# Optimization experiments

Measured on AMD Instinct MI355X. Metric: run time of the kernel, lower is better.

The kernel has to match this reference:

```python
import jax, jax.numpy as jnp
import numpy as np

BINARY_K = 64  # self.binary_k


def setup_inputs() -> dict:
    key = jax.random.key(0)
    ks = jax.random.split(key, 8)
    R, N, D, H = 8, 128, 512, 256
    obj_feats = jax.random.normal(ks[0], (R, N, D), dtype=jnp.float32)
    geo_feats = jax.random.normal(ks[1], (R, N, N, D), dtype=jnp.float32) * 0.1
    mask = jnp.ones((N, N), dtype=jnp.float32)
    mask = mask.at[jnp.arange(N), jnp.arange(N)].set(0.0)  # zero diagonal, as in forward()
    s1 = 1.0 / np.sqrt(D)
    s2 = 1.0 / np.sqrt(H)
    return {
        "obj_feats": obj_feats,
        "geo_feats": geo_feats,
        "mask": mask,
        "w1a": jax.random.normal(ks[2], (D, H), dtype=jnp.float32) * s1,
        "b1a": jnp.zeros((H,), dtype=jnp.float32),
        "w2a": jax.random.normal(ks[3], (H, 1), dtype=jnp.float32) * s2,
        "b2a": jnp.zeros((1,), dtype=jnp.float32),
        "w1b": jax.random.normal(ks[4], (D, H), dtype=jnp.float32) * s1,
        "b1b": jnp.zeros((H,), dtype=jnp.float32),
        "w2b": jax.random.normal(ks[5], (H, 1), dtype=jnp.float32) * s2,
        "b2b": jnp.zeros((1,), dtype=jnp.float32),
    }


def reference(obj_feats, geo_feats, mask, w1a, b1a, w2a, b2a, w1b, b1b, w2b, b2b):
    # pair_aware_perbatch (dropout = identity in eval mode)
    R, N, D = obj_feats.shape
    k = min(BINARY_K, N * N)

    # pairwise outer-product features + geometric features: [R, N, N, D]
    obj2obj = obj_feats[:, None, :, :] * obj_feats[:, :, None, :] + geo_feats

    # re_clf1 MLP scorer: D -> D/2 -> 1
    h = jax.nn.relu(jnp.einsum('rijd,dh->rijh', obj2obj, w1a) + b1a)
    logits = jnp.einsum('rijh,h->rij', h, w2a[:, 0]) + b2a[0]     # [R, N, N]
    o2o_logits = logits.reshape(R, N * N).sum(axis=0) / R          # [N*N]

    pair_probs = jax.nn.sigmoid(o2o_logits) * mask.ravel()
    _, topk_inds = jax.lax.top_k(pair_probs, k)                    # [k]

    # averaged pair features, gather topk
    a_obj2obj = obj2obj.reshape(R, N * N, D).sum(axis=0) / R       # [N*N, D]
    pair_feats = a_obj2obj[topk_inds]                              # [k, D]

    # pair-of-pair outer product + second MLP scorer
    p2p = pair_feats[None, :, :] * pair_feats[:, None, :]          # [k, k, D]
    h2 = jax.nn.relu(jnp.einsum('ijd,dh->ijh', p2p, w1b) + b1b)
    p2p_logits = jnp.einsum('ijh,h->ij', h2, w2b[:, 0]) + b2b[0]   # [k, k]

    return o2o_logits.reshape(N, N), p2p_logits, topk_inds
```

## Files before the change

kernel.cpp:

```cpp
#include <hip/hip_runtime.h>
#include <math.h>

typedef unsigned int u32;
typedef unsigned long long u64;
typedef unsigned short u16;
typedef short bf16x8 __attribute__((ext_vector_type(8)));
typedef float f32x4 __attribute__((ext_vector_type(4)));

#define RR 8
#define NN 128
#define DD 512
#define HH 256
#define KTOP 64
#define NCAND 256
#define NSEL 128

#define WS_LOGITS_OFF 0
#define WS_CAND_OFF   65536
#define WS_EXACT_OFF  66560
#define WS_CNT_OFF    67584
#define WS_TOPK_OFF   67600
#define WS_PF_OFF     67856
#define WS_WH_OFF     198928
#define WS_WL_OFF     461072

__device__ __forceinline__ u16 bf16rne(float x) {
    union { float f; u32 u; } v; v.f = x;
    u32 r = (v.u + 0x7fffu + ((v.u >> 16) & 1u)) >> 16;
    return (u16)r;
}
__device__ __forceinline__ float bf16tof(u16 h) {
    union { float f; u32 u; } v; v.u = ((u32)h) << 16; return v.f;
}
__device__ __forceinline__ u32 f32sort(float x) {
    union { float f; u32 u; } v; v.f = x;
    return v.u ^ ((v.u & 0x80000000u) ? 0xFFFFFFFFu : 0x80000000u);
}

__global__ __launch_bounds__(256) void k0_splitW(const float* __restrict__ W1,
                                                 u16* __restrict__ wh, u16* __restrict__ wl)
{
    const int kc = blockIdx.x;
    const int h  = threadIdx.x;
    const int swz = (h >> 1) & 3;
    u16 rh[32], rl[32];
#pragma unroll
    for (int kk = 0; kk < 32; ++kk) {
        float a = W1[(size_t)(kc * 32 + kk) * HH + h];
        u16 hi = bf16rne(a);
        float lo = a - bf16tof(hi);
        rh[kk] = hi; rl[kk] = bf16rne(lo);
    }
    const size_t base = (size_t)kc * 8192 + (size_t)h * 32;
#pragma unroll
    for (int q = 0; q < 4; ++q) {
        uint4 ph, pl;
        ph.x = (u32)rh[q*8+0] | ((u32)rh[q*8+1] << 16);
        ph.y = (u32)rh[q*8+2] | ((u32)rh[q*8+3] << 16);
        ph.z = (u32)rh[q*8+4] | ((u32)rh[q*8+5] << 16);
        ph.w = (u32)rh[q*8+6] | ((u32)rh[q*8+7] << 16);
        pl.x = (u32)rl[q*8+0] | ((u32)rl[q*8+1] << 16);
        pl.y = (u32)rl[q*8+2] | ((u32)rl[q*8+3] << 16);
        pl.z = (u32)rl[q*8+4] | ((u32)rl[q*8+5] << 16);
        pl.w = (u32)rl[q*8+6] | ((u32)rl[q*8+7] << 16);
        const int qs = (q ^ swz) * 8;
        *(uint4*)&wh[base + qs] = ph;
        *(uint4*)&wl[base + qs] = pl;
    }
}

__global__ __launch_bounds__(256, 2) void k1_pair_mfma(
    const float* __restrict__ obj, const float* __restrict__ geo,
    const u16* __restrict__ wh, const u16* __restrict__ wl,
    const float* __restrict__ b1, const float* __restrict__ w2,
    float* __restrict__ logits_acc)
{
    const int jb = blockIdx.x, i = blockIdx.y, r = blockIdx.z;
    const int j0 = jb * 64;
    const int tid = threadIdx.x;
    const int lane = tid & 63, wv = tid >> 6;
    const int l15 = lane & 15, quad = lane >> 4;
    const int fsl = (quad ^ ((l15 >> 1) & 3)) * 8;

    __shared__ float sObjI[DD];
    __shared__ __align__(16) u16 sAh[64 * 32], sAl[64 * 32];
    __shared__ __align__(16) u16 sBh[256 * 32], sBl[256 * 32];

    const float* objI = obj + (size_t)(r * NN + i) * DD;
    for (int t = tid; t < DD; t += 256) sObjI[t] = objI[t];

    f32x4 acc[4][4];
#pragma unroll
    for (int mt = 0; mt < 4; ++mt)
#pragma unroll
        for (int nt = 0; nt < 4; ++nt) acc[mt][nt] = (f32x4){0.f, 0.f, 0.f, 0.f};

    const float* geoB = geo + ((size_t)(r * NN + i) * NN + j0) * DD;
    const float* objJ = obj + (size_t)(r * NN + j0) * DD;

    const int aj = tid >> 2;
    const int ak = (tid & 3) * 8;
    const int asl = ((tid & 3) ^ ((aj >> 1) & 3)) * 8;

    for (int kc = 0; kc < 16; ++kc) {
        const int k0 = kc * 32;
        __syncthreads();
        {
            const char* gh = (const char*)(wh + (size_t)kc * 8192);
            const char* gl = (const char*)(wl + (size_t)kc * 8192);
#pragma unroll
            for (int p = 0; p < 4; ++p) {
                const int off = (wv * 4 + p) * 1024;
                __builtin_amdgcn_global_load_lds(
                    (const __attribute__((address_space(1))) u32*)(gh + off + lane * 16),
                    (__attribute__((address_space(3))) u32*)((char*)sBh + off), 16, 0, 0);
                __builtin_amdgcn_global_load_lds(
                    (const __attribute__((address_space(1))) u32*)(gl + off + lane * 16),
                    (__attribute__((address_space(3))) u32*)((char*)sBl + off), 16, 0, 0);
            }
        }
        {
            float4 g0 = *(const float4*)(geoB + (size_t)aj * DD + k0 + ak);
            float4 g1 = *(const float4*)(geoB + (size_t)aj * DD + k0 + ak + 4);
            float4 o0 = *(const float4*)(objJ + (size_t)aj * DD + k0 + ak);
            float4 o1 = *(const float4*)(objJ + (size_t)aj * DD + k0 + ak + 4);
            float a[8];
            a[0] = fmaf(sObjI[k0+ak+0], o0.x, g0.x);
            a[1] = fmaf(sObjI[k0+ak+1], o0.y, g0.y);
            a[2] = fmaf(sObjI[k0+ak+2], o0.z, g0.z);
            a[3] = fmaf(sObjI[k0+ak+3], o0.w, g0.w);
            a[4] = fmaf(sObjI[k0+ak+4], o1.x, g1.x);
            a[5] = fmaf(sObjI[k0+ak+5], o1.y, g1.y);
            a[6] = fmaf(sObjI[k0+ak+6], o1.z, g1.z);
            a[7] = fmaf(sObjI[k0+ak+7], o1.w, g1.w);
            u16 hs[8], ls[8];
#pragma unroll
            for (int q = 0; q < 8; ++q) {
                hs[q] = bf16rne(a[q]);
                ls[q] = bf16rne(a[q] - bf16tof(hs[q]));
            }
            uint4 ph, pl;
            ph.x = (u32)hs[0] | ((u32)hs[1] << 16); ph.y = (u32)hs[2] | ((u32)hs[3] << 16);
            ph.z = (u32)hs[4] | ((u32)hs[5] << 16); ph.w = (u32)hs[6] | ((u32)hs[7] << 16);
            pl.x = (u32)ls[0] | ((u32)ls[1] << 16); pl.y = (u32)ls[2] | ((u32)ls[3] << 16);
            pl.z = (u32)ls[4] | ((u32)ls[5] << 16); pl.w = (u32)ls[6] | ((u32)ls[7] << 16);
            *(uint4*)&sAh[aj * 32 + asl] = ph;
            *(uint4*)&sAl[aj * 32 + asl] = pl;
        }
        __syncthreads();
        bf16x8 Bh[4], Bl[4], Ah[4], Al[4];
#pragma unroll
        for (int nt = 0; nt < 4; ++nt) {
            const int row = wv * 64 + nt * 16 + l15;
            Bh[nt] = *(const bf16x8*)&sBh[row * 32 + fsl];
            Bl[nt] = *(const bf16x8*)&sBl[row * 32 + fsl];
        }
#pragma unroll
        for (int mt = 0; mt < 4; ++mt) {
            const int row = mt * 16 + l15;
            Ah[mt] = *(const bf16x8*)&sAh[row * 32 + fsl];
            Al[mt] = *(const bf16x8*)&sAl[row * 32 + fsl];
        }
#pragma unroll
        for (int mt = 0; mt < 4; ++mt)
#pragma unroll
            for (int nt = 0; nt < 4; ++nt) {
                acc[mt][nt] = __builtin_amdgcn_mfma_f32_16x16x32_bf16(Ah[mt], Bh[nt], acc[mt][nt], 0, 0, 0);
                acc[mt][nt] = __builtin_amdgcn_mfma_f32_16x16x32_bf16(Ah[mt], Bl[nt], acc[mt][nt], 0, 0, 0);
                acc[mt][nt] = __builtin_amdgcn_mfma_f32_16x16x32_bf16(Al[mt], Bh[nt], acc[mt][nt], 0, 0, 0);
            }
    }
    float pr[4][4];
#pragma unroll
    for (int mt = 0; mt < 4; ++mt)
#pragma unroll
        for (int t = 0; t < 4; ++t) pr[mt][t] = 0.f;
#pragma unroll
    for (int nt = 0; nt < 4; ++nt) {
        const int h = wv * 64 + nt * 16 + l15;
        const float bb = b1[h], w = w2[h];
#pragma unroll
        for (int mt = 0; mt < 4; ++mt)
#pragma unroll
            for (int t = 0; t < 4; ++t)
                pr[mt][t] += fmaxf(acc[mt][nt][t] + bb, 0.f) * w;
    }
#pragma unroll
    for (int mt = 0; mt < 4; ++mt)
#pragma unroll
        for (int t = 0; t < 4; ++t) {
            float v = pr[mt][t];
            v += __shfl_xor(v, 1); v += __shfl_xor(v, 2);
            v += __shfl_xor(v, 4); v += __shfl_xor(v, 8);
            if (l15 == 0)
                atomicAdd(&logits_acc[i * NN + j0 + mt * 16 + quad * 4 + t], v);
        }
}

__global__ __launch_bounds__(1024) void k2_hist(
    const float* __restrict__ logits_acc, const float* __restrict__ mask,
    const float* __restrict__ b2a, float* __restrict__ out,
    int* __restrict__ cand, int* __restrict__ cnt_out)
{
    __shared__ u32 hist[16 * 256];
    __shared__ u32 sum1[256];
    __shared__ int sB1, sRem, sT16;
    __shared__ u32 sCnt;
    const int t = threadIdx.x;
    const int hb = (t >> 6) << 8;
    for (int b = t; b < 16 * 256; b += 1024) hist[b] = 0;
    if (t == 0) sCnt = 0;
    __syncthreads();
    const float bias = b2a[0];
    u32 skey[16];
#pragma unroll
    for (int e = 0; e < 16; ++e) {
        const int idx = e * 1024 + t;
        const float lg = logits_acc[idx] * 0.125f + bias;
        out[idx] = lg;
        u32 s = f32sort(lg);
        if (mask[idx] == 0.f) s = 0;
        skey[e] = s;
        atomicAdd(&hist[hb + (s >> 24)], 1u);
    }
    __syncthreads();
    if (t < 256) {
        u32 s = 0;
#pragma unroll
        for (int c = 0; c < 16; ++c) s += hist[c * 256 + t];
        sum1[t] = s;
    }
    __syncthreads();
    if (t == 0) {
        u32 cum = 0; int b = 255;
        for (; b > 0; --b) { u32 c = sum1[b]; if (cum + c >= (u32)NSEL) break; cum += c; }
        sB1 = b; sRem = NSEL - (int)cum;
    }
    __syncthreads();
    const int B1 = sB1;
    for (int b = t; b < 16 * 256; b += 1024) hist[b] = 0;
    __syncthreads();
#pragma unroll
    for (int e = 0; e < 16; ++e) {
        const u32 s = skey[e];
        if ((int)(s >> 24) == B1) atomicAdd(&hist[hb + ((s >> 16) & 0xFF)], 1u);
    }
    __syncthreads();
    if (t < 256) {
        u32 s = 0;
#pragma unroll
        for (int c = 0; c < 16; ++c) s += hist[c * 256 + t];
        sum1[t] = s;
    }
    __syncthreads();
    if (t == 0) {
        const int rem = sRem; u32 cum = 0; int b = 255;
        for (; b > 0; --b) { cum += sum1[b]; if ((int)cum >= rem) break; }
        sT16 = (B1 << 8) | b;
    }
    __syncthreads();
    const u32 T16 = (u32)sT16;
#pragma unroll
    for (int e = 0; e < 16; ++e) {
        const u32 s = skey[e];
        if (s != 0 && (s >> 16) >= T16) {
            const u32 pos = atomicAdd(&sCnt, 1u);
            if (pos < (u32)NCAND) cand[pos] = e * 1024 + t;
        }
    }
    __syncthreads();
    if (t == 0) *cnt_out = (int)(sCnt < (u32)NCAND ? sCnt : (u32)NCAND);
}

__global__ __launch_bounds__(256) void k5_exact(
    const float* __restrict__ obj, const float* __restrict__ geo,
    const float* __restrict__ W1, const float* __restrict__ b1,
    const float* __restrict__ w2, const float* __restrict__ b2a,
    const int* __restrict__ cand, const int* __restrict__ cnt_ptr,
    float* __restrict__ exact)
{
    const int c = blockIdx.x;
    if (c >= *cnt_ptr) { if (threadIdx.x == 0) exact[c] = -1e30f; return; }
    const int idx = cand[c];
    const int i = idx >> 7, j = idx & 127;
    const int t = threadIdx.x;
    __shared__ float sA[RR][DD];
    __shared__ float sRed[4];
    for (int f = t; f < RR * DD; f += 256) {
        const int r = f >> 9, k = f & 511;
        sA[r][k] = fmaf(obj[(size_t)(r * NN + i) * DD + k],
                        obj[(size_t)(r * NN + j) * DD + k],
                        geo[((size_t)(r * NN + i) * NN + j) * DD + k]);
    }
    __syncthreads();
    float hv[RR];
#pragma unroll
    for (int r = 0; r < RR; ++r) hv[r] = 0.f;
#pragma unroll 4
    for (int k = 0; k < DD; ++k) {
        const float w = W1[(size_t)k * HH + t];
#pragma unroll
        for (int r = 0; r < RR; ++r) hv[r] = fmaf(sA[r][k], w, hv[r]);
    }
    const float bb = b1[t], wv2 = w2[t];
    float p = 0.f;
#pragma unroll
    for (int r = 0; r < RR; ++r) p += fmaxf(hv[r] + bb, 0.f) * wv2;
#pragma unroll
    for (int off = 1; off < 64; off <<= 1) p += __shfl_xor(p, off);
    if ((t & 63) == 0) sRed[t >> 6] = p;
    __syncthreads();
    if (t == 0) exact[c] = (sRed[0] + sRed[1] + sRed[2] + sRed[3]) * 0.125f + b2a[0];
}

__global__ __launch_bounds__(256) void k_sort(
    const float* __restrict__ exact, const int* __restrict__ cand,
    float* __restrict__ out, int* __restrict__ topk)
{
    __shared__ u64 sKey[NCAND];
    const int t = threadIdx.x;
    {
        const float lg = exact[t];
        u32 ps = 0; u32 idx = 0x7FFFFFFFu;
        if (lg > -1e29f) {
            const float p = 1.f / (1.f + expf(-lg));
            ps = f32sort(p);
            idx = (u32)cand[t];
        }
        sKey[t] = ((u64)ps << 32) | (u64)(0xFFFFFFFFu - idx);
    }
    for (int k = 2; k <= NCAND; k <<= 1)
        for (int j = k >> 1; j > 0; j >>= 1) {
            __syncthreads();
            const int ixj = t ^ j;
            if (ixj > t) {
                const u64 a = sKey[t], b = sKey[ixj];
                if (((t & k) == 0) ? (a < b) : (a > b)) { sKey[t] = b; sKey[ixj] = a; }
            }
        }
    __syncthreads();
    if (t < KTOP) {
        const u32 idx = 0xFFFFFFFFu - (u32)(sKey[t] & 0xFFFFFFFFull);
        topk[t] = (int)idx;
        out[20480 + t] = (float)idx;
    }
}

__global__ __launch_bounds__(256) void k3_gather(
    const float* __restrict__ obj, const float* __restrict__ geo,
    const int* __restrict__ ws_topk, float* __restrict__ pf)
{
    const int tix = blockIdx.x;
    const int idx = ws_topk[tix];
    const int i = idx >> 7, j = idx & 127;
    for (int dd = threadIdx.x; dd < DD; dd += 256) {
        float s = 0.f;
#pragma unroll
        for (int r = 0; r < RR; ++r) {
            const float oi = obj[(size_t)(r * NN + i) * DD + dd];
            const float oj = obj[(size_t)(r * NN + j) * DD + dd];
            const float g  = geo[((size_t)(r * NN + i) * NN + j) * DD + dd];
            s += oi * oj + g;
        }
        pf[tix * DD + dd] = s * 0.125f;
    }
}

__global__ __launch_bounds__(256) void k4_p2p(
    const float* __restrict__ pf, const float* __restrict__ W1,
    const float* __restrict__ b1, const float* __restrict__ w2,
    const float* __restrict__ b2, float* __restrict__ out)
{
    const int a = blockIdx.x;
    const int tid = threadIdx.x;
    const int tx = tid & 15, ty = tid >> 4;

    __shared__ float sPfA[DD];
    __shared__ __align__(16) float sA[32][68];
    __shared__ __align__(16) float sB[32][HH];

    const float* pfA = pf + (size_t)a * DD;
    for (int t = tid; t < DD; t += 256) sPfA[t] = pfA[t];

    float acc[4][16];
#pragma unroll
    for (int m = 0; m < 4; ++m)
#pragma unroll
        for (int n = 0; n < 16; ++n) acc[m][n] = 0.f;

    for (int kc = 0; kc < 16; ++kc) {
        const int k0 = kc * 32;
        __syncthreads();
#pragma unroll
        for (int p = 0; p < 8; ++p) {
            const int f = tid + p * 256;
            const int kk = f >> 6, c = (f & 63) << 2;
            *(float4*)&sB[kk][c] = *(const float4*)&W1[(size_t)(k0 + kk) * HH + c];
        }
#pragma unroll
        for (int p = 0; p < 2; ++p) {
            const int f = tid + p * 256;
            const int j = f >> 3, kk = (f & 7) << 2;
            float4 o = *(const float4*)(pf + (size_t)j * DD + k0 + kk);
            sA[kk + 0][j] = sPfA[k0 + kk + 0] * o.x;
            sA[kk + 1][j] = sPfA[k0 + kk + 1] * o.y;
            sA[kk + 2][j] = sPfA[k0 + kk + 2] * o.z;
            sA[kk + 3][j] = sPfA[k0 + kk + 3] * o.w;
        }
        __syncthreads();
#pragma unroll 8
        for (int kk = 0; kk < 32; ++kk) {
            float4 a4 = *(const float4*)&sA[kk][ty << 2];
            float av[4] = {a4.x, a4.y, a4.z, a4.w};
#pragma unroll
            for (int n4 = 0; n4 < 4; ++n4) {
                float4 b4 = *(const float4*)&sB[kk][(n4 << 6) + (tx << 2)];
                float bv[4] = {b4.x, b4.y, b4.z, b4.w};
#pragma unroll
                for (int m = 0; m < 4; ++m)
#pragma unroll
                    for (int c = 0; c < 4; ++c)
                        acc[m][(n4 << 2) + c] = fmaf(av[m], bv[c], acc[m][(n4 << 2) + c]);
            }
        }
    }
    const float b20 = b2[0];
    float pr[4] = {0.f, 0.f, 0.f, 0.f};
#pragma unroll
    for (int n4 = 0; n4 < 4; ++n4)
#pragma unroll
        for (int c = 0; c < 4; ++c) {
            const int h = (n4 << 6) + (tx << 2) + c;
            const float bb = b1[h], w = w2[h];
#pragma unroll
            for (int m = 0; m < 4; ++m)
                pr[m] += fmaxf(acc[m][(n4 << 2) + c] + bb, 0.f) * w;
        }
#pragma unroll
    for (int m = 0; m < 4; ++m) {
        pr[m] += __shfl_xor(pr[m], 1); pr[m] += __shfl_xor(pr[m], 2);
        pr[m] += __shfl_xor(pr[m], 4); pr[m] += __shfl_xor(pr[m], 8);
        if (tx == 0)
            out[16384 + a * 64 + (ty << 2) + m] = pr[m] + b20;
    }
}

extern "C" void kernel_launch(void* const* d_in, const int* in_sizes, int n_in,
                              void* d_out, int out_size, void* d_ws, size_t ws_size,
                              hipStream_t stream) {
    const float* obj  = (const float*)d_in[0];
    const float* geo  = (const float*)d_in[1];
    const float* mask = (const float*)d_in[2];
    const float* w1a  = (const float*)d_in[3];
    const float* b1a  = (const float*)d_in[4];
    const float* w2a  = (const float*)d_in[5];
    const float* b2a  = (const float*)d_in[6];
    const float* w1b  = (const float*)d_in[7];
    const float* b1b  = (const float*)d_in[8];
    const float* w2b  = (const float*)d_in[9];
    const float* b2b  = (const float*)d_in[10];
    float* out = (float*)d_out;

    char* ws = (char*)d_ws;
    float* ws_logits = (float*)(ws + WS_LOGITS_OFF);
    int*   ws_cand   = (int*)  (ws + WS_CAND_OFF);
    float* ws_exact  = (float*)(ws + WS_EXACT_OFF);
    int*   ws_cnt    = (int*)  (ws + WS_CNT_OFF);
    int*   ws_topk   = (int*)  (ws + WS_TOPK_OFF);
    float* ws_pf     = (float*)(ws + WS_PF_OFF);
    u16*   ws_wh     = (u16*)  (ws + WS_WH_OFF);
    u16*   ws_wl     = (u16*)  (ws + WS_WL_OFF);

    hipMemsetAsync(ws_logits, 0, 16384 * sizeof(float), stream);

    k0_splitW<<<16, 256, 0, stream>>>(w1a, ws_wh, ws_wl);
    k1_pair_mfma<<<dim3(2, NN, RR), 256, 0, stream>>>(obj, geo, ws_wh, ws_wl, b1a, w2a, ws_logits);
    k2_hist<<<1, 1024, 0, stream>>>(ws_logits, mask, b2a, out, ws_cand, ws_cnt);
    k5_exact<<<NCAND, 256, 0, stream>>>(obj, geo, w1a, b1a, w2a, b2a, ws_cand, ws_cnt, ws_exact);
    k_sort<<<1, 256, 0, stream>>>(ws_exact, ws_cand, out, ws_topk);
    k3_gather<<<KTOP, 256, 0, stream>>>(obj, geo, ws_topk, ws_pf);
    k4_p2p<<<KTOP, 256, 0, stream>>>(ws_pf, w1b, b1b, w2b, b2b, out);
}
```

Baseline: 636.8 us.

## Software-pipeline weight staging and activation loads across K chunks

Restructures the main GEMM K-loop so the next chunk's geo and obj loads are issued into registers before the current chunk is converted and stored. The next chunk's weight tiles are also started into LDS right after the current fragments are read, so global latency overlaps the MFMA work. The full __syncthreads calls are replaced by explicit waitcnt plus s_barrier, with partial vmcnt waits so the prefetches can stay in flight. MFMA sections are wrapped in s_setprio to favour matrix issue. The risk is that the hand-written vmcnt counts depend on the compiler keeping the exact load count and order, and the prefetch raises register pressure.

```diff
diff --git a/kernel.cpp b/kernel.cpp
--- a/kernel.cpp
+++ b/kernel.cpp
@@ -102,37 +102,49 @@
     const int ak = (tid & 3) * 8;
     const int asl = ((tid & 3) ^ ((aj >> 1) & 3)) * 8;
 
+#define STAGE_B(KC) do { \
+    const char* gh_ = (const char*)(wh + (size_t)(KC) * 8192); \
+    const char* gl_ = (const char*)(wl + (size_t)(KC) * 8192); \
+    _Pragma("unroll") \
+    for (int p_ = 0; p_ < 4; ++p_) { \
+        const int off_ = (wv * 4 + p_) * 1024; \
+        __builtin_amdgcn_global_load_lds( \
+            (const __attribute__((address_space(1))) u32*)(gh_ + off_ + lane * 16), \
+            (__attribute__((address_space(3))) u32*)((char*)sBh + off_), 16, 0, 0); \
+        __builtin_amdgcn_global_load_lds( \
+            (const __attribute__((address_space(1))) u32*)(gl_ + off_ + lane * 16), \
+            (__attribute__((address_space(3))) u32*)((char*)sBl + off_), 16, 0, 0); \
+    } \
+} while (0)
+
+    STAGE_B(0);
+    float4 g0 = *(const float4*)(geoB + (size_t)aj * DD + ak);
+    float4 g1 = *(const float4*)(geoB + (size_t)aj * DD + ak + 4);
+    float4 o0 = *(const float4*)(objJ + (size_t)aj * DD + ak);
+    float4 o1 = *(const float4*)(objJ + (size_t)aj * DD + ak + 4);
+    asm volatile("s_waitcnt lgkmcnt(0)" ::: "memory");
+    __builtin_amdgcn_s_barrier();
+
+#pragma unroll 1
     for (int kc = 0; kc < 16; ++kc) {
         const int k0 = kc * 32;
-        __syncthreads();
+        float a[8];
+        a[0] = fmaf(sObjI[k0+ak+0], o0.x, g0.x);
+        a[1] = fmaf(sObjI[k0+ak+1], o0.y, g0.y);
+        a[2] = fmaf(sObjI[k0+ak+2], o0.z, g0.z);
+        a[3] = fmaf(sObjI[k0+ak+3], o0.w, g0.w);
+        a[4] = fmaf(sObjI[k0+ak+4], o1.x, g1.x);
+        a[5] = fmaf(sObjI[k0+ak+5], o1.y, g1.y);
+        a[6] = fmaf(sObjI[k0+ak+6], o1.z, g1.z);
+        a[7] = fmaf(sObjI[k0+ak+7], o1.w, g1.w);
         {
-            const char* gh = (const char*)(wh + (size_t)kc * 8192);
-            const char* gl = (const char*)(wl + (size_t)kc * 8192);
-#pragma unroll
-            for (int p = 0; p < 4; ++p) {
-                const int off = (wv * 4 + p) * 1024;
-                __builtin_amdgcn_global_load_lds(
-                    (const __attribute__((address_space(1))) u32*)(gh + off + lane * 16),
-                    (__attribute__((address_space(3))) u32*)((char*)sBh + off), 16, 0, 0);
-                __builtin_amdgcn_global_load_lds(
-                    (const __attribute__((address_space(1))) u32*)(gl + off + lane * 16),
-                    (__attribute__((address_space(3))) u32*)((char*)sBl + off), 16, 0, 0);
-            }
+            const int kp = (kc < 15) ? (kc + 1) * 32 : 15 * 32;
+            const float* gp = geoB + (size_t)aj * DD + kp + ak;
+            const float* op = objJ + (size_t)aj * DD + kp + ak;
+            g0 = *(const float4*)gp;  g1 = *(const float4*)(gp + 4);
+            o0 = *(const float4*)op;  o1 = *(const float4*)(op + 4);
         }
         {
-            float4 g0 = *(const float4*)(geoB + (size_t)aj * DD + k0 + ak);
-            float4 g1 = *(const float4*)(geoB + (size_t)aj * DD + k0 + ak + 4);
-            float4 o0 = *(const float4*)(objJ + (size_t)aj * DD + k0 + ak);
-            float4 o1 = *(const float4*)(objJ + (size_t)aj * DD + k0 + ak + 4);
-            float a[8];
-            a[0] = fmaf(sObjI[k0+ak+0], o0.x, g0.x);
-            a[1] = fmaf(sObjI[k0+ak+1], o0.y, g0.y);
-            a[2] = fmaf(sObjI[k0+ak+2], o0.z, g0.z);
-            a[3] = fmaf(sObjI[k0+ak+3], o0.w, g0.w);
-            a[4] = fmaf(sObjI[k0+ak+4], o1.x, g1.x);
-            a[5] = fmaf(sObjI[k0+ak+5], o1.y, g1.y);
-            a[6] = fmaf(sObjI[k0+ak+6], o1.z, g1.z);
-            a[7] = fmaf(sObjI[k0+ak+7], o1.w, g1.w);
             u16 hs[8], ls[8];
 #pragma unroll
             for (int q = 0; q < 8; ++q) {
@@ -147,7 +159,8 @@
             *(uint4*)&sAh[aj * 32 + asl] = ph;
             *(uint4*)&sAl[aj * 32 + asl] = pl;
         }
-        __syncthreads();
+        asm volatile("s_waitcnt vmcnt(4) lgkmcnt(0)" ::: "memory");
+        __builtin_amdgcn_s_barrier();
         bf16x8 Bh[4], Bl[4], Ah[4], Al[4];
 #pragma unroll
         for (int nt = 0; nt < 4; ++nt) {
@@ -161,6 +174,10 @@
             Ah[mt] = *(const bf16x8*)&sAh[row * 32 + fsl];
             Al[mt] = *(const bf16x8*)&sAl[row * 32 + fsl];
         }
+        asm volatile("s_waitcnt lgkmcnt(0)" ::: "memory");
+        __builtin_amdgcn_s_barrier();
+        if (kc < 15) STAGE_B(kc + 1);
+        __builtin_amdgcn_s_setprio(1);
 #pragma unroll
         for (int mt = 0; mt < 4; ++mt)
 #pragma unroll
@@ -169,7 +186,10 @@
                 acc[mt][nt] = __builtin_amdgcn_mfma_f32_16x16x32_bf16(Ah[mt], Bl[nt], acc[mt][nt], 0, 0, 0);
                 acc[mt][nt] = __builtin_amdgcn_mfma_f32_16x16x32_bf16(Al[mt], Bh[nt], acc[mt][nt], 0, 0, 0);
             }
-    }
+        __builtin_amdgcn_s_setprio(0);
+    }
+#undef STAGE_B
+
     float pr[4][4];
 #pragma unroll
     for (int mt = 0; mt < 4; ++mt)
```

Result: no change. 635.4 us (-0.2%).
